# Kernel tuning notes

Measured on AMD Instinct MI355X. Metric: run time of the kernel, lower is better.

The kernel has to match this reference:

```python
import jax, jax.numpy as jnp
import numpy as np

N, C_IN, C_OUT, H, RANK = 16, 4, 32, 400, 4


def setup_inputs() -> dict:
    key = jax.random.key(0)
    k1, k2, k3 = jax.random.split(key, 3)
    x = jax.random.normal(k1, (N, C_IN, H, H), dtype=jnp.float32)
    # symmetric sylo: weight_R tied to weight_L (shape C_out x C_in x H x rank)
    fan_in = C_IN * H
    scale = 1.0 / np.sqrt(fan_in)
    weight_L = jax.random.normal(k2, (C_OUT, C_IN, H, RANK), dtype=jnp.float32) * scale
    bias = jax.random.uniform(k3, (C_OUT,), dtype=jnp.float32, minval=-scale, maxval=scale)
    return {"x": x, "weight_L": weight_L, "bias": bias}


def reference(x, weight_L, bias):
    # Expand low-rank symmetric template: T[o,c] = L[o,c] @ L[o,c].T  (H x H)
    T = jnp.einsum('ocir,ocjr->ocij', weight_L, weight_L)
    # Crosshair similarity, summed over input channels:
    # out[n,o,i,j] = sum_c [ sum_k X[n,c,i,k]T[o,c,i,k] + sum_k X[n,c,k,j]T[o,c,k,j] - X[n,c,i,j]T[o,c,i,j] ]
    rows = jnp.einsum('ncik,ocik->noi', x, T)   # row sums of X*T
    cols = jnp.einsum('nckj,ockj->noj', x, T)   # column sums of X*T
    diag = jnp.einsum('ncij,ocij->noij', x, T)  # pointwise term (counted twice)
    out = rows[..., :, None] + cols[..., None, :] - diag
    return out + bias[None, :, None, None]
```

## Files before the change

### kernel.cpp

```cpp
#include <hip/hip_runtime.h>

#define H  400
#define NB 16
#define CI 4
#define CO 32

__global__ __launch_bounds__(256) void k_transpose(const float* __restrict__ x,
                                                   float* __restrict__ xt) {
    __shared__ float tile[50][51];
    int b = blockIdx.x;
    int tj = b & 7;
    int ti = (b >> 3) & 7;
    int nc = b >> 6;
    const float* src = x + (size_t)nc * H * H;
    float* dst = xt + (size_t)nc * H * H;
    int i0 = ti * 50, j0 = tj * 50;
    for (int e = threadIdx.x; e < 2500; e += 256) {
        int r = e / 50, c = e % 50;
        tile[r][c] = src[(i0 + r) * H + j0 + c];
    }
    __syncthreads();
    for (int e = threadIdx.x; e < 2500; e += 256) {
        int r = e / 50, c = e % 50;
        dst[(j0 + r) * H + i0 + c] = tile[c][r];
    }
}

#define KC 40
__global__ __launch_bounds__(256) void k_rowscols(const float* __restrict__ x,
        const float* __restrict__ xcol, int xt_flag, const float* __restrict__ L,
        float* __restrict__ rows, float* __restrict__ cols)
{
    __shared__ __align__(16) float Lm[CO * CI * 4];
    __shared__ __align__(16) float Xr[NB * CI * KC];
    __shared__ __align__(16) float Xc[NB * CI * KC];
    __shared__ __align__(16) float Tr[CO * 164];
    int m = blockIdx.x;
    int tid = threadIdx.x;
    const float4* L4 = (const float4*)L;
    if (tid < CO * CI) ((float4*)Lm)[tid] = L4[tid * H + m];

    int o  = tid & 31;
    int n0 = tid >> 5;
    int n1 = n0 + 8;
    float ar0 = 0.f, ar1 = 0.f, ac0 = 0.f, ac1 = 0.f;

    for (int ch = 0; ch < H / KC; ++ch) {
        int k0 = ch * KC;
        __syncthreads();
        for (int e = tid; e < NB * CI * KC; e += 256) {
            int k = e % KC;
            int nc = e / KC;
            Xr[e] = x[(nc * H + m) * H + k0 + k];
            Xc[e] = xt_flag ? xcol[(nc * H + m) * H + k0 + k]
                            : xcol[(nc * H + k0 + k) * H + m];
        }
        for (int e = tid; e < CO * CI * KC; e += 256) {
            int k = e % KC;
            int oc = e / KC;
            float4 lv = L4[oc * H + k0 + k];
            float4 lm = ((const float4*)Lm)[oc];
            Tr[(oc >> 2) * 164 + (oc & 3) * KC + k] =
                lv.x * lm.x + lv.y * lm.y + lv.z * lm.z + lv.w * lm.w;
        }
        __syncthreads();
        #pragma unroll
        for (int c = 0; c < CI; ++c) {
            const float4* trp = (const float4*)(Tr + o * 164 + c * KC);
            const float4* pr0 = (const float4*)(Xr + (n0 * CI + c) * KC);
            const float4* pr1 = (const float4*)(Xr + (n1 * CI + c) * KC);
            const float4* pc0 = (const float4*)(Xc + (n0 * CI + c) * KC);
            const float4* pc1 = (const float4*)(Xc + (n1 * CI + c) * KC);
            #pragma unroll
            for (int q = 0; q < KC / 4; ++q) {
                float4 tv = trp[q];
                float4 a  = pr0[q];
                float4 bb = pr1[q];
                float4 cc = pc0[q];
                float4 dd = pc1[q];
                ar0 += tv.x * a.x  + tv.y * a.y  + tv.z * a.z  + tv.w * a.w;
                ar1 += tv.x * bb.x + tv.y * bb.y + tv.z * bb.z + tv.w * bb.w;
                ac0 += tv.x * cc.x + tv.y * cc.y + tv.z * cc.z + tv.w * cc.w;
                ac1 += tv.x * dd.x + tv.y * dd.y + tv.z * dd.z + tv.w * dd.w;
            }
        }
    }
    rows[(n0 * CO + o) * H + m] = ar0;
    rows[(n1 * CO + o) * H + m] = ar1;
    cols[(n0 * CO + o) * H + m] = ac0;
    cols[(n1 * CO + o) * H + m] = ac1;
}

#define TS 16
__global__ __launch_bounds__(512) void k_out(const float* __restrict__ x,
        const float* __restrict__ L, const float* __restrict__ bias,
        const float* __restrict__ rows, const float* __restrict__ cols,
        float* __restrict__ out)
{
    __shared__ __align__(16) float Xl[NB * CI * TS * TS];
    __shared__ __align__(16) float rT[NB * 8 * TS];
    __shared__ __align__(16) float cT[NB * 8 * TS];
    int b = blockIdx.x;
    int os = b / 625;
    int t  = b % 625;
    int ti = t / 25, tj = t % 25;
    int i0 = ti * TS, j0 = tj * TS, ob = os * 8;
    int tid = threadIdx.x;

    for (int e = tid; e < NB * 8 * TS; e += 512) {
        int ii = e & 15;
        int o  = (e >> 4) & 7;
        int n  = e >> 7;
        rT[e] = rows[(n * CO + ob + o) * H + i0 + ii];
        cT[e] = cols[(n * CO + ob + o) * H + j0 + ii];
    }
    const float4* x4 = (const float4*)x;
    float4* Xl4 = (float4*)Xl;
    for (int e = tid; e < NB * CI * TS * 4; e += 512) {
        int q  = e & 3;
        int ii = (e >> 2) & 15;
        int nc = e >> 6;
        Xl4[e] = x4[(nc * H + i0 + ii) * 100 + tj * 4 + q];
    }

    int o  = tid >> 6;
    int u  = tid & 63;
    int ii = u >> 2, jq = u & 3;
    int og = ob + o;
    const float4* L4 = (const float4*)L;
    float4 T4[CI];
    #pragma unroll
    for (int c = 0; c < CI; ++c) {
        float4 Li = L4[(og * CI + c) * H + i0 + ii];
        float4 La = L4[(og * CI + c) * H + j0 + jq * 4 + 0];
        float4 Lb = L4[(og * CI + c) * H + j0 + jq * 4 + 1];
        float4 Lc = L4[(og * CI + c) * H + j0 + jq * 4 + 2];
        float4 Ld = L4[(og * CI + c) * H + j0 + jq * 4 + 3];
        T4[c].x = Li.x * La.x + Li.y * La.y + Li.z * La.z + Li.w * La.w;
        T4[c].y = Li.x * Lb.x + Li.y * Lb.y + Li.z * Lb.z + Li.w * Lb.w;
        T4[c].z = Li.x * Lc.x + Li.y * Lc.y + Li.z * Lc.z + Li.w * Lc.w;
        T4[c].w = Li.x * Ld.x + Li.y * Ld.y + Li.z * Ld.z + Li.w * Ld.w;
    }
    float bo = bias[og];
    __syncthreads();

    const float4* cT4 = (const float4*)cT;
    float4* out4 = (float4*)out;
    for (int n = 0; n < NB; ++n) {
        float ra = rT[(n * 8 + o) * TS + ii] + bo;
        float4 ca = cT4[(n * 8 + o) * 4 + jq];
        float4 acc;
        acc.x = ra + ca.x; acc.y = ra + ca.y; acc.z = ra + ca.z; acc.w = ra + ca.w;
        #pragma unroll
        for (int c = 0; c < CI; ++c) {
            float4 xv = Xl4[((n * CI + c) * TS + ii) * 4 + jq];
            acc.x -= xv.x * T4[c].x;
            acc.y -= xv.y * T4[c].y;
            acc.z -= xv.z * T4[c].z;
            acc.w -= xv.w * T4[c].w;
        }
        out4[((n * CO + og) * H + i0 + ii) * 100 + tj * 4 + jq] = acc;
    }
}

extern "C" void kernel_launch(void* const* d_in, const int* in_sizes, int n_in,
                              void* d_out, int out_size, void* d_ws, size_t ws_size,
                              hipStream_t stream) {
    const float* x    = (const float*)d_in[0];
    const float* L    = (const float*)d_in[1];
    const float* bias = (const float*)d_in[2];
    float* out = (float*)d_out;
    char* ws = (char*)d_ws;

    size_t xt_bytes = (size_t)NB * CI * H * H * sizeof(float);
    size_t rc_elems = (size_t)NB * CO * H;
    size_t rc_bytes = rc_elems * sizeof(float);

    int use_xt = (ws_size >= xt_bytes + 2 * rc_bytes);
    float* XT;
    float* rows;
    float* cols;
    if (use_xt) {
        XT   = (float*)ws;
        rows = (float*)(ws + xt_bytes);
        cols = rows + rc_elems;
    } else {
        XT   = nullptr;
        rows = (float*)ws;
        cols = rows + rc_elems;
    }

    if (use_xt) {
        k_transpose<<<4096, 256, 0, stream>>>(x, XT);
        k_rowscols<<<H, 256, 0, stream>>>(x, XT, 1, L, rows, cols);
    } else {
        k_rowscols<<<H, 256, 0, stream>>>(x, x, 0, L, rows, cols);
    }
    k_out<<<2500, 512, 0, stream>>>(x, L, bias, rows, cols, out);
}
```

Before: 551.5 us.

## Split rowscols reduction over K, vectorize transpose, and loop output channels in k_out

The row/column sum kernel is split five ways along the reduction dimension, so it launches 2000 blocks instead of 400. Partial sums go to a workspace and are combined by a new reduce kernel. The transpose now uses 80x80 tiles with float4 global loads and stores. k_out now loops over the four output-channel groups inside each block, so the x tile is loaded once and reused across all channels. The workspace-size fallback is removed, so the code assumes enough workspace, and the extra launch plus partial-sum traffic add cost.

Result: faster. 509.2 us (-7.7%).

```diff
diff --git a/kernel.cpp b/kernel.cpp
--- a/kernel.cpp
+++ b/kernel.cpp
@@ -5,61 +5,69 @@
 #define CI 4
 #define CO 32
 
+#define TT 80
 __global__ __launch_bounds__(256) void k_transpose(const float* __restrict__ x,
                                                    float* __restrict__ xt) {
-    __shared__ float tile[50][51];
+    __shared__ float tile[TT][TT + 5];
     int b = blockIdx.x;
-    int tj = b & 7;
-    int ti = (b >> 3) & 7;
-    int nc = b >> 6;
+    int tj = b % 5;
+    int ti = (b / 5) % 5;
+    int nc = b / 25;
     const float* src = x + (size_t)nc * H * H;
     float* dst = xt + (size_t)nc * H * H;
-    int i0 = ti * 50, j0 = tj * 50;
-    for (int e = threadIdx.x; e < 2500; e += 256) {
-        int r = e / 50, c = e % 50;
-        tile[r][c] = src[(i0 + r) * H + j0 + c];
+    int i0 = ti * TT, j0 = tj * TT;
+    for (int e = threadIdx.x; e < TT * 20; e += 256) {
+        int r = e / 20, q = e % 20;
+        float4 v = ((const float4*)(src + (size_t)(i0 + r) * H + j0))[q];
+        tile[r][q * 4 + 0] = v.x; tile[r][q * 4 + 1] = v.y;
+        tile[r][q * 4 + 2] = v.z; tile[r][q * 4 + 3] = v.w;
     }
     __syncthreads();
-    for (int e = threadIdx.x; e < 2500; e += 256) {
-        int r = e / 50, c = e % 50;
-        dst[(j0 + r) * H + i0 + c] = tile[c][r];
+    for (int e = threadIdx.x; e < TT * 20; e += 256) {
+        int r = e / 20, q = e % 20;
+        float4 v;
+        v.x = tile[q * 4 + 0][r]; v.y = tile[q * 4 + 1][r];
+        v.z = tile[q * 4 + 2][r]; v.w = tile[q * 4 + 3][r];
+        ((float4*)(dst + (size_t)(j0 + r) * H + i0))[q] = v;
     }
 }
 
 #define KC 40
+#define KSPLIT 5
 __global__ __launch_bounds__(256) void k_rowscols(const float* __restrict__ x,
-        const float* __restrict__ xcol, int xt_flag, const float* __restrict__ L,
-        float* __restrict__ rows, float* __restrict__ cols)
+        const float* __restrict__ xt, const float* __restrict__ L,
+        float* __restrict__ rowsP, float* __restrict__ colsP)
 {
-    __shared__ __align__(16) float Lm[CO * CI * 4];
+    __shared__ __align__(16) float4 Lm[CO * CI];
     __shared__ __align__(16) float Xr[NB * CI * KC];
     __shared__ __align__(16) float Xc[NB * CI * KC];
     __shared__ __align__(16) float Tr[CO * 164];
-    int m = blockIdx.x;
+    int b = blockIdx.x;
+    int m  = b / KSPLIT;
+    int ks = b % KSPLIT;
     int tid = threadIdx.x;
     const float4* L4 = (const float4*)L;
-    if (tid < CO * CI) ((float4*)Lm)[tid] = L4[tid * H + m];
+    if (tid < CO * CI) Lm[tid] = L4[tid * H + m];
 
     int o  = tid & 31;
     int n0 = tid >> 5;
     int n1 = n0 + 8;
     float ar0 = 0.f, ar1 = 0.f, ac0 = 0.f, ac1 = 0.f;
 
-    for (int ch = 0; ch < H / KC; ++ch) {
-        int k0 = ch * KC;
-        __syncthreads();
-        for (int e = tid; e < NB * CI * KC; e += 256) {
-            int k = e % KC;
-            int nc = e / KC;
-            Xr[e] = x[(nc * H + m) * H + k0 + k];
-            Xc[e] = xt_flag ? xcol[(nc * H + m) * H + k0 + k]
-                            : xcol[(nc * H + k0 + k) * H + m];
+    for (int ch = 0; ch < 2; ++ch) {
+        int k0 = ks * 80 + ch * KC;
+        __syncthreads();
+        for (int e = tid; e < NB * CI * KC / 4; e += 256) {
+            int q  = e % 10;
+            int nc = e / 10;
+            ((float4*)Xr)[e] = *(const float4*)(x  + (size_t)(nc * H + m) * H + k0 + q * 4);
+            ((float4*)Xc)[e] = *(const float4*)(xt + (size_t)(nc * H + m) * H + k0 + q * 4);
         }
         for (int e = tid; e < CO * CI * KC; e += 256) {
-            int k = e % KC;
+            int k  = e % KC;
             int oc = e / KC;
             float4 lv = L4[oc * H + k0 + k];
-            float4 lm = ((const float4*)Lm)[oc];
+            float4 lm = Lm[oc];
             Tr[(oc >> 2) * 164 + (oc & 3) * KC + k] =
                 lv.x * lm.x + lv.y * lm.y + lv.z * lm.z + lv.w * lm.w;
         }
@@ -85,10 +93,27 @@
             }
         }
     }
-    rows[(n0 * CO + o) * H + m] = ar0;
-    rows[(n1 * CO + o) * H + m] = ar1;
-    cols[(n0 * CO + o) * H + m] = ac0;
-    cols[(n1 * CO + o) * H + m] = ac1;
+    size_t base = (size_t)ks * NB * CO * H;
+    rowsP[base + (size_t)(n0 * CO + o) * H + m] = ar0;
+    rowsP[base + (size_t)(n1 * CO + o) * H + m] = ar1;
+    colsP[base + (size_t)(n0 * CO + o) * H + m] = ac0;
+    colsP[base + (size_t)(n1 * CO + o) * H + m] = ac1;
+}
+
+__global__ __launch_bounds__(256) void k_reduce(const float* __restrict__ rowsP,
+        const float* __restrict__ colsP, float* __restrict__ rows, float* __restrict__ cols)
+{
+    int i = blockIdx.x * 256 + threadIdx.x;
+    if (i < NB * CO * H) {
+        float s = 0.f, t = 0.f;
+        #pragma unroll
+        for (int k = 0; k < KSPLIT; ++k) {
+            s += rowsP[(size_t)k * NB * CO * H + i];
+            t += colsP[(size_t)k * NB * CO * H + i];
+        }
+        rows[i] = s;
+        cols[i] = t;
+    }
 }
 
 #define TS 16
@@ -101,65 +126,68 @@
     __shared__ __align__(16) float rT[NB * 8 * TS];
     __shared__ __align__(16) float cT[NB * 8 * TS];
     int b = blockIdx.x;
-    int os = b / 625;
-    int t  = b % 625;
-    int ti = t / 25, tj = t % 25;
-    int i0 = ti * TS, j0 = tj * TS, ob = os * 8;
+    int ti = b / 25, tj = b % 25;
+    int i0 = ti * TS, j0 = tj * TS;
     int tid = threadIdx.x;
 
-    for (int e = tid; e < NB * 8 * TS; e += 512) {
-        int ii = e & 15;
-        int o  = (e >> 4) & 7;
-        int n  = e >> 7;
-        rT[e] = rows[(n * CO + ob + o) * H + i0 + ii];
-        cT[e] = cols[(n * CO + ob + o) * H + j0 + ii];
-    }
     const float4* x4 = (const float4*)x;
     float4* Xl4 = (float4*)Xl;
     for (int e = tid; e < NB * CI * TS * 4; e += 512) {
         int q  = e & 3;
         int ii = (e >> 2) & 15;
         int nc = e >> 6;
-        Xl4[e] = x4[(nc * H + i0 + ii) * 100 + tj * 4 + q];
+        Xl4[e] = x4[(size_t)(nc * H + i0 + ii) * 100 + tj * 4 + q];
     }
 
     int o  = tid >> 6;
     int u  = tid & 63;
     int ii = u >> 2, jq = u & 3;
-    int og = ob + o;
     const float4* L4 = (const float4*)L;
-    float4 T4[CI];
-    #pragma unroll
-    for (int c = 0; c < CI; ++c) {
-        float4 Li = L4[(og * CI + c) * H + i0 + ii];
-        float4 La = L4[(og * CI + c) * H + j0 + jq * 4 + 0];
-        float4 Lb = L4[(og * CI + c) * H + j0 + jq * 4 + 1];
-        float4 Lc = L4[(og * CI + c) * H + j0 + jq * 4 + 2];
-        float4 Ld = L4[(og * CI + c) * H + j0 + jq * 4 + 3];
-        T4[c].x = Li.x * La.x + Li.y * La.y + Li.z * La.z + Li.w * La.w;
-        T4[c].y = Li.x * Lb.x + Li.y * Lb.y + Li.z * Lb.z + Li.w * Lb.w;
-        T4[c].z = Li.x * Lc.x + Li.y * Lc.y + Li.z * Lc.z + Li.w * Lc.w;
-        T4[c].w = Li.x * Ld.x + Li.y * Ld.y + Li.z * Ld.z + Li.w * Ld.w;
-    }
-    float bo = bias[og];
-    __syncthreads();
-
     const float4* cT4 = (const float4*)cT;
     float4* out4 = (float4*)out;
-    for (int n = 0; n < NB; ++n) {
-        float ra = rT[(n * 8 + o) * TS + ii] + bo;
-        float4 ca = cT4[(n * 8 + o) * 4 + jq];
-        float4 acc;
-        acc.x = ra + ca.x; acc.y = ra + ca.y; acc.z = ra + ca.z; acc.w = ra + ca.w;
+
+    for (int os = 0; os < 4; ++os) {
+        int og = os * 8 + o;
+        float4 T4[CI];
         #pragma unroll
         for (int c = 0; c < CI; ++c) {
-            float4 xv = Xl4[((n * CI + c) * TS + ii) * 4 + jq];
-            acc.x -= xv.x * T4[c].x;
-            acc.y -= xv.y * T4[c].y;
-            acc.z -= xv.z * T4[c].z;
-            acc.w -= xv.w * T4[c].w;
-        }
-        out4[((n * CO + og) * H + i0 + ii) * 100 + tj * 4 + jq] = acc;
+            float4 Li = L4[(og * CI + c) * H + i0 + ii];
+            float4 La = L4[(og * CI + c) * H + j0 + jq * 4 + 0];
+            float4 Lb = L4[(og * CI + c) * H + j0 + jq * 4 + 1];
+            float4 Lc = L4[(og * CI + c) * H + j0 + jq * 4 + 2];
+            float4 Ld = L4[(og * CI + c) * H + j0 + jq * 4 + 3];
+            T4[c].x = Li.x * La.x + Li.y * La.y + Li.z * La.z + Li.w * La.w;
+            T4[c].y = Li.x * Lb.x + Li.y * Lb.y + Li.z * Lb.z + Li.w * Lb.w;
+            T4[c].z = Li.x * Lc.x + Li.y * Lc.y + Li.z * Lc.z + Li.w * Lc.w;
+            T4[c].w = Li.x * Ld.x + Li.y * Ld.y + Li.z * Ld.z + Li.w * Ld.w;
+        }
+        float bo = bias[og];
+
+        __syncthreads();
+        for (int e = tid; e < NB * 8 * TS; e += 512) {
+            int iw = e & 15;
+            int oo = (e >> 4) & 7;
+            int n  = e >> 7;
+            rT[e] = rows[(size_t)(n * CO + os * 8 + oo) * H + i0 + iw];
+            cT[e] = cols[(size_t)(n * CO + os * 8 + oo) * H + j0 + iw];
+        }
+        __syncthreads();
+
+        for (int n = 0; n < NB; ++n) {
+            float ra = rT[(n * 8 + o) * TS + ii] + bo;
+            float4 ca = cT4[(n * 8 + o) * 4 + jq];
+            float4 acc;
+            acc.x = ra + ca.x; acc.y = ra + ca.y; acc.z = ra + ca.z; acc.w = ra + ca.w;
+            #pragma unroll
+            for (int c = 0; c < CI; ++c) {
+                float4 xv = Xl4[((n * CI + c) * TS + ii) * 4 + jq];
+                acc.x -= xv.x * T4[c].x;
+                acc.y -= xv.y * T4[c].y;
+                acc.z -= xv.z * T4[c].z;
+                acc.w -= xv.w * T4[c].w;
+            }
+            out4[((size_t)(n * CO + og) * H + i0 + ii) * 100 + tj * 4 + jq] = acc;
+        }
     }
 }
 
@@ -174,27 +202,18 @@
 
     size_t xt_bytes = (size_t)NB * CI * H * H * sizeof(float);
     size_t rc_elems = (size_t)NB * CO * H;
-    size_t rc_bytes = rc_elems * sizeof(float);
-
-    int use_xt = (ws_size >= xt_bytes + 2 * rc_bytes);
-    float* XT;
-    float* rows;
-    float* cols;
-    if (use_xt) {
-        XT   = (float*)ws;
-        rows = (float*)(ws + xt_bytes);
-        cols = rows + rc_elems;
-    } else {
-        XT   = nullptr;
-        rows = (float*)ws;
-        cols = rows + rc_elems;
-    }
-
-    if (use_xt) {
-        k_transpose<<<4096, 256, 0, stream>>>(x, XT);
-        k_rowscols<<<H, 256, 0, stream>>>(x, XT, 1, L, rows, cols);
-    } else {
-        k_rowscols<<<H, 256, 0, stream>>>(x, x, 0, L, rows, cols);
-    }
-    k_out<<<2500, 512, 0, stream>>>(x, L, bias, rows, cols, out);
-}
+    size_t rcP_bytes = (size_t)KSPLIT * rc_elems * sizeof(float);
+    size_t rc_bytes  = rc_elems * sizeof(float);
+
+    float* XT    = (float*)ws;
+    float* rowsP = (float*)(ws + xt_bytes);
+    float* colsP = (float*)(ws + xt_bytes + rcP_bytes);
+    float* rows  = (float*)(ws + xt_bytes + 2 * rcP_bytes);
+    float* cols  = (float*)(ws + xt_bytes + 2 * rcP_bytes + rc_bytes);
+    (void)ws_size;
+
+    k_transpose<<<1600, 256, 0, stream>>>(x, XT);
+    k_rowscols<<<H * KSPLIT, 256, 0, stream>>>(x, XT, L, rowsP, colsP);
+    k_reduce<<<(NB * CO * H + 255) / 256, 256, 0, stream>>>(rowsP, colsP, rows, cols);
+    k_out<<<625, 512, 0, stream>>>(x, L, bias, rows, cols, out);
+}
```
